# Kernel tuning notes

Measured on AMD Instinct MI355X. Metric: run time of the kernel, lower is better.

Reference implementation:

```python
import jax, jax.numpy as jnp
import numpy as np

N = 50000
IN_CHNL = 128
OUT_CHNL = 64
HEADS = 2
NEG_SLOPE = 0.2  # PyG GATConv default leaky_relu slope


def gat_conv(x, W, a_src, a_dst, bias, edge_index):
    """PyG-style GATConv (concat=True, add_self_loops=True, eval mode).
    x: [N, F_in], W: [F_in, H*C], a_src/a_dst: [H, C], bias: [H*C],
    edge_index: [2, E] (row 0 = src, row 1 = dst)."""
    n = x.shape[0]
    loops = jnp.arange(n, dtype=edge_index.dtype)
    src = jnp.concatenate([edge_index[0], loops])
    dst = jnp.concatenate([edge_index[1], loops])

    h = (x @ W).reshape(n, HEADS, OUT_CHNL)          # [N, H, C]
    s_src = jnp.einsum('nhc,hc->nh', h, a_src)       # [N, H]
    s_dst = jnp.einsum('nhc,hc->nh', h, a_dst)       # [N, H]

    e = s_src[src] + s_dst[dst]                      # [E', H]
    e = jax.nn.leaky_relu(e, NEG_SLOPE)
    # segment softmax over destination neighborhoods
    e_max = jax.ops.segment_max(e, dst, num_segments=n)
    e_max = jnp.where(jnp.isfinite(e_max), e_max, 0.0)
    e_exp = jnp.exp(e - e_max[dst])
    denom = jax.ops.segment_sum(e_exp, dst, num_segments=n)
    alpha = e_exp / denom[dst]                       # [E', H]

    msg = h[src] * alpha[:, :, None]                 # [E', H, C]
    out = jax.ops.segment_sum(msg, dst, num_segments=n)  # [N, H, C]
    return out.reshape(n, HEADS * OUT_CHNL) + bias


def setup_inputs() -> dict:
    key = jax.random.key(0)
    ks = jax.random.split(key, 12)
    node_h = jax.random.normal(ks[0], (N, IN_CHNL), dtype=jnp.float32)
    edge_index_pc = jax.random.randint(ks[1], (2, 600000), 0, N, dtype=jnp.int64 if jax.config.jax_enable_x64 else jnp.int32)
    edge_index_mc = jax.random.randint(ks[2], (2, 600000), 0, N, dtype=jnp.int64 if jax.config.jax_enable_x64 else jnp.int32)
    sc = 1.0 / np.sqrt(IN_CHNL)
    W_pc = jax.random.normal(ks[3], (IN_CHNL, HEADS * OUT_CHNL), dtype=jnp.float32) * sc
    a_src_pc = jax.random.normal(ks[4], (HEADS, OUT_CHNL), dtype=jnp.float32) * sc
    a_dst_pc = jax.random.normal(ks[5], (HEADS, OUT_CHNL), dtype=jnp.float32) * sc
    b_pc = jnp.zeros((HEADS * OUT_CHNL,), dtype=jnp.float32)
    W_mc = jax.random.normal(ks[6], (IN_CHNL, HEADS * OUT_CHNL), dtype=jnp.float32) * sc
    a_src_mc = jax.random.normal(ks[7], (HEADS, OUT_CHNL), dtype=jnp.float32) * sc
    a_dst_mc = jax.random.normal(ks[8], (HEADS, OUT_CHNL), dtype=jnp.float32) * sc
    b_mc = jnp.zeros((HEADS * OUT_CHNL,), dtype=jnp.float32)
    return {
        'node_h': node_h,
        'W_pc': W_pc, 'a_src_pc': a_src_pc, 'a_dst_pc': a_dst_pc, 'b_pc': b_pc,
        'W_mc': W_mc, 'a_src_mc': a_src_mc, 'a_dst_mc': a_dst_mc, 'b_mc': b_mc,
        'edge_index_pc': edge_index_pc, 'edge_index_mc': edge_index_mc,
    }


def reference(node_h, W_pc, a_src_pc, a_dst_pc, b_pc,
              W_mc, a_src_mc, a_dst_mc, b_mc,
              edge_index_pc, edge_index_mc):
    # eval mode: F.dropout is identity
    h_pc = jax.nn.elu(gat_conv(node_h, W_pc, a_src_pc, a_dst_pc, b_pc, edge_index_pc))
    h_mc = jax.nn.elu(gat_conv(node_h, W_mc, a_src_mc, a_dst_mc, b_mc, edge_index_mc))
    return 0.5 * (h_pc + h_mc)
```

## Files before the change

### kernel.cpp

```cpp
#include <hip/hip_runtime.h>
#include <hip/hip_bf16.h>

typedef unsigned int u32;
typedef unsigned short u16;
typedef long long i64;
typedef __bf16 bf16x8 __attribute__((ext_vector_type(8)));
typedef float f32x4 __attribute__((ext_vector_type(4)));

static constexpr int NN = 50000;
static constexpr int FI = 128;
static constexpr int FO = 128;
static constexpr int ER = 600000;
static constexpr int GLAB = 6272;
static constexpr int PROWS = 12544;
static constexpr int DSTRIDE = 38;
static constexpr int NQA = 1280;
static constexpr int ACS = (2 * ER + NQA - 1) / NQA;
static constexpr int NBIN = 128;
static constexpr int RBLK = 784;
static constexpr int LCAP = 24;
static constexpr int QCAPB = 10240;
static constexpr int GEMM_BLK = (NN + 63) / 64;
static constexpr int NGEMM = 2 * GEMM_BLK;
static constexpr float SLOPE = 0.2f;

__device__ __forceinline__ float bf2f(u16 u) {
  u32 x = ((u32)u) << 16;
  return __builtin_bit_cast(float, x);
}
__device__ __forceinline__ u16 f2bf(float f) {
  u32 u = __builtin_bit_cast(u32, f);
  u32 r = (u + 0x7fffu + ((u >> 16) & 1u)) >> 16;
  return (u16)r;
}
__device__ __forceinline__ float ldf(const void* p, size_t i, int isf32) {
  return isf32 ? ((const float*)p)[i] : bf2f(((const u16*)p)[i]);
}
__device__ __forceinline__ int lde(const void* p, size_t i, int is64) {
  return is64 ? (int)((const i64*)p)[i] : ((const int*)p)[i];
}

__global__ void wfrag_prep(const void* __restrict__ W0,
                           const void* __restrict__ W1,
                           const u32* __restrict__ x,
                           const u32* __restrict__ ei, u16* __restrict__ wf,
                           int* __restrict__ flags, int* __restrict__ qcurp) {
  int lane = threadIdx.x;
  u32 e = (x[lane] >> 23) & 0xffu;
  unsigned long long b1 = __ballot(e >= 118u && e <= 137u);
  int f32i = (__popcll(b1) >= 48) ? 1 : 0;
  int bid = blockIdx.x;
  if (bid == 64) {
    u32 hi = (lane < 32) ? ei[2 * lane + 1] : 1u;
    unsigned long long b2 = __ballot(hi == 0u);
    if (lane == 0) {
      flags[0] = f32i;
      flags[1] = (__popcll(b2) >= 30) ? 1 : 0;
    }
    for (int i = lane; i < NBIN * 16; i += 64) qcurp[i] = 0;
    return;
  }
  int g = bid >> 5, idx = bid & 31;
  const void* W = g ? W1 : W0;
  int ks = idx >> 3, cg = idx & 7;
  int k0 = ks * 32 + (lane >> 4) * 8;
  int col = cg * 16 + (lane & 15);
  u16 v[8];
#pragma unroll
  for (int j = 0; j < 8; j++) v[j] = f2bf(ldf(W, (size_t)(k0 + j) * FO + col, f32i));
  u32 p0 = (u32)v[0] | ((u32)v[1] << 16);
  u32 p1 = (u32)v[2] | ((u32)v[3] << 16);
  u32 p2 = (u32)v[4] | ((u32)v[5] << 16);
  u32 p3 = (u32)v[6] | ((u32)v[7] << 16);
  *reinterpret_cast<uint4*>(wf + (size_t)(bid * 64 + lane) * 8) =
      make_uint4(p0, p1, p2, p3);
}

__device__ __forceinline__ void passA_body(const void* __restrict__ ei0,
                                           const void* __restrict__ ei1,
                                           int* __restrict__ qcurp,
                                           u32* __restrict__ qbuf, int bid) {
  __shared__ u32 lq[NBIN][LCAP];
  __shared__ int lcnt[NBIN];
  __shared__ int gbase[NBIN];
  __shared__ int s_i64;
  int tid = threadIdx.x;
  if (tid < NBIN) lcnt[tid] = 0;
  if (tid < 64) {
    u32 hi = (tid < 32) ? ((const u32*)ei0)[2 * tid + 1] : 1u;
    unsigned long long b2 = __ballot(hi == 0u);
    if (tid == 0) s_i64 = (__popcll(b2) >= 30) ? 1 : 0;
  }
  __syncthreads();
  int i64f = s_i64;
  int beg = bid * ACS;
  int end = min(beg + ACS, 2 * ER);
  for (int e = beg + tid; e < end; e += 256) {
    int g = e >= ER;
    int ee = e - g * ER;
    const void* ei = g ? ei1 : ei0;
    int d = lde(ei, (size_t)ER + ee, i64f);
    int s = lde(ei, (size_t)ee, i64f);
    s = min(max(s, 0), NN - 1);
    d = min(max(d, 0), NN - 1);
    int p = d & 7;
    int label = (d >> 3) + g * GLAB;
    int r = label / RBLK;
    int bin = p * 16 + r;
    int ll = label - r * RBLK;
    u32 entry = ((u32)s << 16) | (u32)ll;
    int pos = atomicAdd(&lcnt[bin], 1);
    if (pos < LCAP) {
      lq[bin][pos] = entry;
    } else {
      int idx = atomicAdd(&qcurp[bin * 16], 1);
      if (idx < QCAPB) qbuf[(size_t)bin * QCAPB + idx] = entry;
    }
  }
  __syncthreads();
  if (tid < NBIN) {
    int n = min(lcnt[tid], LCAP);
    lcnt[tid] = n;
    gbase[tid] = atomicAdd(&qcurp[tid * 16], n);
  }
  __syncthreads();
  int wv = tid >> 6, lane = tid & 63;
  for (int b = wv; b < NBIN; b += 4) {
    int n = lcnt[b];
    int gb = gbase[b];
    for (int i = lane; i < n; i += 64) {
      int idx = gb + i;
      if (idx < QCAPB) qbuf[(size_t)b * QCAPB + idx] = lq[b][i];
    }
  }
}

__device__ __forceinline__ void gemm_body(
    const void* __restrict__ x, const u16* __restrict__ wf,
    u16* __restrict__ h0, u16* __restrict__ h1, const void* __restrict__ as0,
    const void* __restrict__ ad0, const void* __restrict__ as1,
    const void* __restrict__ ad1, float* __restrict__ ss,
    float* __restrict__ sd, int f32i, int gb) {
  int g = gb >= GEMM_BLK;
  int bid = gb - g * GEMM_BLK;
  u16* h = g ? h1 : h0;
  const void* as = g ? as1 : as0;
  const void* ad = g ? ad1 : ad0;
  int tid = threadIdx.x;
  int lane = tid & 63, wv = tid >> 6;
  int rowbase = bid * 64 + wv * 16;
  int arow = rowbase + (lane & 15);
  if (arow >= NN) arow = NN - 1;
  int kg = lane >> 4;

  f32x4 acc[8];
#pragma unroll
  for (int i = 0; i < 8; i++) acc[i] = (f32x4){0.f, 0.f, 0.f, 0.f};

#pragma unroll
  for (int ks = 0; ks < 4; ks++) {
    uint4 q;
    if (f32i) {
      const float* xp = (const float*)x + (size_t)arow * FI + ks * 32 + kg * 8;
      float4 v0 = *reinterpret_cast<const float4*>(xp);
      float4 v1 = *reinterpret_cast<const float4*>(xp + 4);
      q.x = (u32)f2bf(v0.x) | ((u32)f2bf(v0.y) << 16);
      q.y = (u32)f2bf(v0.z) | ((u32)f2bf(v0.w) << 16);
      q.z = (u32)f2bf(v1.x) | ((u32)f2bf(v1.y) << 16);
      q.w = (u32)f2bf(v1.z) | ((u32)f2bf(v1.w) << 16);
    } else {
      q = *reinterpret_cast<const uint4*>((const u16*)x + (size_t)arow * FI +
                                          ks * 32 + kg * 8);
    }
    bf16x8 a = __builtin_bit_cast(bf16x8, q);
#pragma unroll
    for (int cg = 0; cg < 8; cg++) {
      bf16x8 b = __builtin_bit_cast(
          bf16x8, *reinterpret_cast<const uint4*>(
                      wf + (size_t)((g * 32 + ks * 8 + cg) * 64 + lane) * 8));
      acc[cg] = __builtin_amdgcn_mfma_f32_16x16x32_bf16(a, b, acc[cg], 0, 0, 0);
    }
  }
#pragma unroll
  for (int cg = 0; cg < 8; cg++) {
#pragma unroll
    for (int r = 0; r < 4; r++) {
      int orow = rowbase + kg * 4 + r;
      if (orow < NN)
        h[(size_t)orow * FO + cg * 16 + (lane & 15)] = f2bf(acc[cg][r]);
    }
  }
  float sa[2][4], sb[2][4];
#pragma unroll
  for (int i = 0; i < 2; i++)
#pragma unroll
    for (int r = 0; r < 4; r++) {
      sa[i][r] = 0.f;
      sb[i][r] = 0.f;
    }
#pragma unroll
  for (int cg = 0; cg < 8; cg++) {
    int c = cg * 16 + (lane & 15);
    float av = ldf(as, c, f32i);
    float dv = ldf(ad, c, f32i);
    int ih = cg >> 2;
#pragma unroll
    for (int r = 0; r < 4; r++) {
      sa[ih][r] += acc[cg][r] * av;
      sb[ih][r] += acc[cg][r] * dv;
    }
  }
#pragma unroll
  for (int i = 0; i < 2; i++)
#pragma unroll
    for (int r = 0; r < 4; r++)
#pragma unroll
      for (int off = 1; off <= 8; off <<= 1) {
        sa[i][r] += __shfl_xor(sa[i][r], off, 64);
        sb[i][r] += __shfl_xor(sb[i][r], off, 64);
      }
  if ((lane & 15) < 4) {
    int r = lane & 3;
    int row = rowbase + kg * 4 + r;
    if (row < NN) {
      reinterpret_cast<float2*>(ss)[(size_t)g * NN + row] =
          make_float2(sa[0][r], sa[1][r]);
      reinterpret_cast<float2*>(sd)[(size_t)g * NN + row] =
          make_float2(sb[0][r], sb[1][r]);
    }
  }
}

__global__ __launch_bounds__(256) void fat1(
    const void* __restrict__ x, const u16* __restrict__ wf,
    u16* __restrict__ h0, u16* __restrict__ h1, const void* __restrict__ as0,
    const void* __restrict__ ad0, const void* __restrict__ as1,
    const void* __restrict__ ad1, float* __restrict__ ss,
    float* __restrict__ sd, const void* __restrict__ ei0,
    const void* __restrict__ ei1, int* __restrict__ qcurp,
    u32* __restrict__ qbuf, const int* __restrict__ flags) {
  if (blockIdx.x < NGEMM) {
    gemm_body(x, wf, h0, h1, as0, ad0, as1, ad1, ss, sd, flags[0],
              blockIdx.x);
  } else {
    passA_body(ei0, ei1, qcurp, qbuf, blockIdx.x - NGEMM);
  }
}

__global__ __launch_bounds__(256) void passB(const int* __restrict__ qcurp,
                                             const u32* __restrict__ qbuf,
                                             int* __restrict__ deg,
                                             u16* __restrict__ slots) {
  __shared__ int ldeg[RBLK];
  __shared__ u16 lslots[RBLK * DSTRIDE];
  int tid = threadIdx.x;
  int bin = blockIdx.x;
  int p = bin >> 4, r = bin & 15;
  for (int i = tid; i < RBLK; i += 256) {
    int lgl = r * RBLK + i;
    int g = lgl >= GLAB;
    int lg = lgl - g * GLAB;
    int dst = (lg << 3) | p;
    if (dst < NN) {
      ldeg[i] = 1;
      lslots[i * DSTRIDE] = (u16)dst;
    } else {
      ldeg[i] = 0;
    }
  }
  __syncthreads();
  int qn = min(qcurp[bin * 16], QCAPB);
  const u32* q = qbuf + (size_t)bin * QCAPB;
  for (int i = tid; i < qn; i += 256) {
    u32 pr = q[i];
    int ll = (int)(pr & 0xffffu);
    int old = atomicAdd(&ldeg[ll], 1);
    if (old < DSTRIDE) lslots[ll * DSTRIDE + old] = (u16)(pr >> 16);
  }
  __syncthreads();
  int rowbase = p * PROWS + r * RBLK;
  for (int i = tid; i < RBLK; i += 256) deg[rowbase + i] = min(ldeg[i], DSTRIDE);
  const u32* ls32 = reinterpret_cast<const u32*>(lslots);
  u32* gs32 = reinterpret_cast<u32*>(slots + (size_t)rowbase * DSTRIDE);
  for (int i = tid; i < RBLK * DSTRIDE / 2; i += 256) gs32[i] = ls32[i];
}

__global__ __launch_bounds__(256) void agg2(
    const u16* __restrict__ h0, const u16* __restrict__ h1,
    const float* __restrict__ ss, const float* __restrict__ sd,
    const int* __restrict__ deg, const u16* __restrict__ slots,
    const void* __restrict__ b0p, const void* __restrict__ b1p,
    void* __restrict__ outp, const int* __restrict__ flags) {
  int f32i = flags[0];
  int tid = threadIdx.x;
  int lane = tid & 63, wv = tid >> 6;
  int half = lane >> 5;
  int c = lane & 31;
  int dst = blockIdx.x * 8 + wv * 2 + half;
  int head = c >> 4;
  int hsh = head << 4;
  int hbase = half << 5;
  float res[2][4];
#pragma unroll
  for (int g = 0; g < 2; g++) {
    const uint2* hw = reinterpret_cast<const uint2*>(g ? h1 : h0);
    const float2* ss2 = reinterpret_cast<const float2*>(ss) + (size_t)g * NN;
    float2 sdv = reinterpret_cast<const float2*>(sd)[(size_t)g * NN + dst];
    int row = (dst & 7) * PROWS + g * GLAB + (dst >> 3);
    int n = min(deg[row], DSTRIDE);
    const u16* srow = slots + (size_t)row * DSTRIDE;
    int n1 = min(n, 32);
    int s1 = 0, s2 = 0;
    u32 pp1 = 0, pp2 = 0;
    float dp0 = 0.f, dp1 = 0.f;
    if (c < n1) {
      s1 = srow[c];
      float2 sv = ss2[s1];
      float e0 = sv.x + sdv.x, e1 = sv.y + sdv.y;
      e0 = (e0 > 0.f) ? e0 : SLOPE * e0;
      e1 = (e1 > 0.f) ? e1 : SLOPE * e1;
      float q0 = __expf(e0), q1 = __expf(e1);
      pp1 = (u32)f2bf(q0) | ((u32)f2bf(q1) << 16);
      dp0 += q0;
      dp1 += q1;
    }
    if (c + 32 < n) {
      s2 = srow[c + 32];
      float2 sv = ss2[s2];
      float e0 = sv.x + sdv.x, e1 = sv.y + sdv.y;
      e0 = (e0 > 0.f) ? e0 : SLOPE * e0;
      e1 = (e1 > 0.f) ? e1 : SLOPE * e1;
      float q0 = __expf(e0), q1 = __expf(e1);
      pp2 = (u32)f2bf(q0) | ((u32)f2bf(q1) << 16);
      dp0 += q0;
      dp1 += q1;
    }
#pragma unroll
    for (int off = 16; off >= 1; off >>= 1) {
      dp0 += __shfl_xor(dp0, off, 32);
      dp1 += __shfl_xor(dp1, off, 32);
    }
    float den = head ? dp1 : dp0;
    float a0 = 0.f, a1 = 0.f, a2 = 0.f, a3 = 0.f;
    int n1full = n1 & ~7;
    for (int b = 0; b < n1full; b += 8) {
      uint2 hv[8];
      float pv[8];
#pragma unroll
      for (int t = 0; t < 8; t++) {
        int sj = __shfl(s1, hbase + b + t, 64);
        u32 pp = __shfl(pp1, hbase + b + t, 64);
        pv[t] = bf2f((u16)(pp >> hsh));
        hv[t] = hw[(size_t)sj * 32 + c];
      }
#pragma unroll
      for (int t = 0; t < 8; t++) {
        a0 += pv[t] * bf2f((u16)hv[t].x);
        a1 += pv[t] * bf2f((u16)(hv[t].x >> 16));
        a2 += pv[t] * bf2f((u16)hv[t].y);
        a3 += pv[t] * bf2f((u16)(hv[t].y >> 16));
      }
    }
    if (n1full < n1) {
      uint2 hv[8];
      float pv[8];
#pragma unroll
      for (int t = 0; t < 8; t++) {
        int jj = (n1full + t < n1) ? (n1full + t) : n1full;
        int sj = __shfl(s1, hbase + jj, 64);
        u32 pp = __shfl(pp1, hbase + jj, 64);
        pv[t] = (n1full + t < n1) ? bf2f((u16)(pp >> hsh)) : 0.f;
        hv[t] = hw[(size_t)sj * 32 + c];
      }
#pragma unroll
      for (int t = 0; t < 8; t++) {
        a0 += pv[t] * bf2f((u16)hv[t].x);
        a1 += pv[t] * bf2f((u16)(hv[t].x >> 16));
        a2 += pv[t] * bf2f((u16)hv[t].y);
        a3 += pv[t] * bf2f((u16)(hv[t].y >> 16));
      }
    }
    if (n > 32) {
      int n2 = n - 32;
      for (int b = 0; b < n2; b += 8) {
        uint2 hv[8];
        float pv[8];
#pragma unroll
        for (int t = 0; t < 8; t++) {
          int jj = (b + t < n2) ? (b + t) : b;
          int sj = __shfl(s2, hbase + jj, 64);
          u32 pp = __shfl(pp2, hbase + jj, 64);
          pv[t] = (b + t < n2) ? bf2f((u16)(pp >> hsh)) : 0.f;
          hv[t] = hw[(size_t)sj * 32 + c];
        }
#pragma unroll
        for (int t = 0; t < 8; t++) {
          a0 += pv[t] * bf2f((u16)hv[t].x);
          a1 += pv[t] * bf2f((u16)(hv[t].x >> 16));
          a2 += pv[t] * bf2f((u16)hv[t].y);
          a3 += pv[t] * bf2f((u16)(hv[t].y >> 16));
        }
      }
    }
    float inv = (den > 0.f) ? 1.0f / den : 0.f;
    const void* bias = g ? b1p : b0p;
    float r0 = a0 * inv + ldf(bias, 4 * c + 0, f32i);
    float r1 = a1 * inv + ldf(bias, 4 * c + 1, f32i);
    float r2 = a2 * inv + ldf(bias, 4 * c + 2, f32i);
    float r3 = a3 * inv + ldf(bias, 4 * c + 3, f32i);
    res[g][0] = (r0 > 0.f) ? r0 : (__expf(r0) - 1.0f);
    res[g][1] = (r1 > 0.f) ? r1 : (__expf(r1) - 1.0f);
    res[g][2] = (r2 > 0.f) ? r2 : (__expf(r2) - 1.0f);
    res[g][3] = (r3 > 0.f) ? r3 : (__expf(r3) - 1.0f);
  }
  float r0 = 0.5f * (res[0][0] + res[1][0]);
  float r1 = 0.5f * (res[0][1] + res[1][1]);
  float r2 = 0.5f * (res[0][2] + res[1][2]);
  float r3 = 0.5f * (res[0][3] + res[1][3]);
  if (f32i) {
    reinterpret_cast<float4*>(outp)[(size_t)dst * 32 + c] =
        make_float4(r0, r1, r2, r3);
  } else {
    uint2 o;
    o.x = (u32)f2bf(r0) | ((u32)f2bf(r1) << 16);
    o.y = (u32)f2bf(r2) | ((u32)f2bf(r3) << 16);
    reinterpret_cast<uint2*>(outp)[(size_t)dst * 32 + c] = o;
  }
}

extern "C" void kernel_launch(void* const* d_in, const int* in_sizes, int n_in,
                              void* d_out, int out_size, void* d_ws, size_t ws_size,
                              hipStream_t stream) {
  (void)in_sizes; (void)n_in; (void)out_size; (void)ws_size;
  const void* x = d_in[0];

  char* base = (char*)d_ws;
  size_t off = 0;
  auto alloc = [&](size_t bytes) -> void* {
    void* p = base + off;
    off = (off + bytes + 255) & ~(size_t)255;
    return p;
  };
  int* flags = (int*)alloc(16);
  int* qcurp = (int*)alloc((size_t)NBIN * 16 * 4);
  u16* h0    = (u16*)alloc((size_t)NN * FO * 2);
  u16* h1    = (u16*)alloc((size_t)NN * FO * 2);
  float* ss  = (float*)alloc((size_t)2 * NN * 2 * 4);
  float* sd  = (float*)alloc((size_t)2 * NN * 2 * 4);
  u16* wf    = (u16*)alloc((size_t)2 * 32 * 64 * 8 * 2);
  int* deg   = (int*)alloc((size_t)8 * PROWS * 4);
  u16* slots = (u16*)alloc((size_t)8 * PROWS * DSTRIDE * 2);
  u32* qbuf  = (u32*)alloc((size_t)NBIN * QCAPB * 4);

  const int AGG_BLK = NN / 8;

  wfrag_prep<<<65, 64, 0, stream>>>(d_in[1], d_in[5], (const u32*)x,
                                    (const u32*)d_in[9], wf, flags, qcurp);
  fat1<<<NGEMM + NQA, 256, 0, stream>>>(x, wf, h0, h1, d_in[2], d_in[3],
                                        d_in[6], d_in[7], ss, sd, d_in[9],
                                        d_in[10], qcurp, qbuf, flags);
  passB<<<NBIN, 256, 0, stream>>>(qcurp, qbuf, deg, slots);
  agg2<<<AGG_BLK, 256, 0, stream>>>(h0, h1, ss, sd, deg, slots, d_in[4],
                                    d_in[8], d_out, flags);
}
```

Before: 130.5 us.

## Store h in column-permuted layout with vectorized 16-byte writes, unpermute in aggregation

The GEMM epilogue now writes each output row of h as one packed 16-byte store per lane, which permutes the column order of h, instead of scattering eight separate 2-byte stores. The aggregation kernel adapts to that layout: head selection becomes c&1, bias columns are remapped, and the final results go through shared memory to restore the original column order before the coalesced output store. This is meant to cut scattered write traffic in the GEMM, at the cost of an LDS round-trip per output row in the aggregation kernel.

```diff
diff --git a/kernel.cpp b/kernel.cpp
--- a/kernel.cpp
+++ b/kernel.cpp
@@ -23,6 +23,7 @@
 static constexpr int GEMM_BLK = (NN + 63) / 64;
 static constexpr int NGEMM = 2 * GEMM_BLK;
 static constexpr float SLOPE = 0.2f;
+
 
 __device__ __forceinline__ float bf2f(u16 u) {
   u32 x = ((u32)u) << 16;
@@ -181,13 +182,20 @@
       acc[cg] = __builtin_amdgcn_mfma_f32_16x16x32_bf16(a, b, acc[cg], 0, 0, 0);
     }
   }
-#pragma unroll
-  for (int cg = 0; cg < 8; cg++) {
-#pragma unroll
-    for (int r = 0; r < 4; r++) {
-      int orow = rowbase + kg * 4 + r;
-      if (orow < NN)
-        h[(size_t)orow * FO + cg * 16 + (lane & 15)] = f2bf(acc[cg][r]);
+  int c15 = lane & 15;
+#pragma unroll
+  for (int r = 0; r < 4; r++) {
+    int orow = rowbase + kg * 4 + r;
+    if (orow < NN) {
+      u16 v[8];
+#pragma unroll
+      for (int cg = 0; cg < 8; cg++) v[cg] = f2bf(acc[cg][r]);
+      uint4 q4;
+      q4.x = (u32)v[0] | ((u32)v[1] << 16);
+      q4.y = (u32)v[2] | ((u32)v[3] << 16);
+      q4.z = (u32)v[4] | ((u32)v[5] << 16);
+      q4.w = (u32)v[6] | ((u32)v[7] << 16);
+      *reinterpret_cast<uint4*>(h + (size_t)orow * FO + c15 * 8) = q4;
     }
   }
   float sa[2][4], sb[2][4];
@@ -200,7 +208,7 @@
     }
 #pragma unroll
   for (int cg = 0; cg < 8; cg++) {
-    int c = cg * 16 + (lane & 15);
+    int c = cg * 16 + c15;
     float av = ldf(as, c, f32i);
     float dv = ldf(ad, c, f32i);
     int ih = cg >> 2;
@@ -219,7 +227,7 @@
         sa[i][r] += __shfl_xor(sa[i][r], off, 64);
         sb[i][r] += __shfl_xor(sb[i][r], off, 64);
       }
-  if ((lane & 15) < 4) {
+  if (c15 < 4) {
     int r = lane & 3;
     int row = rowbase + kg * 4 + r;
     if (row < NN) {
@@ -291,13 +299,14 @@
     const int* __restrict__ deg, const u16* __restrict__ slots,
     const void* __restrict__ b0p, const void* __restrict__ b1p,
     void* __restrict__ outp, const int* __restrict__ flags) {
+  __shared__ float xbuf[4][2][128];
   int f32i = flags[0];
   int tid = threadIdx.x;
   int lane = tid & 63, wv = tid >> 6;
   int half = lane >> 5;
   int c = lane & 31;
   int dst = blockIdx.x * 8 + wv * 2 + half;
-  int head = c >> 4;
+  int head = c & 1;
   int hsh = head << 4;
   int hbase = half << 5;
   float res[2][4];
@@ -404,26 +413,34 @@
     }
     float inv = (den > 0.f) ? 1.0f / den : 0.f;
     const void* bias = g ? b1p : b0p;
-    float r0 = a0 * inv + ldf(bias, 4 * c + 0, f32i);
-    float r1 = a1 * inv + ldf(bias, 4 * c + 1, f32i);
-    float r2 = a2 * inv + ldf(bias, 4 * c + 2, f32i);
-    float r3 = a3 * inv + ldf(bias, 4 * c + 3, f32i);
-    res[g][0] = (r0 > 0.f) ? r0 : (__expf(r0) - 1.0f);
-    res[g][1] = (r1 > 0.f) ? r1 : (__expf(r1) - 1.0f);
-    res[g][2] = (r2 > 0.f) ? r2 : (__expf(r2) - 1.0f);
-    res[g][3] = (r3 > 0.f) ? r3 : (__expf(r3) - 1.0f);
-  }
-  float r0 = 0.5f * (res[0][0] + res[1][0]);
-  float r1 = 0.5f * (res[0][1] + res[1][1]);
-  float r2 = 0.5f * (res[0][2] + res[1][2]);
-  float r3 = 0.5f * (res[0][3] + res[1][3]);
+    float aa[4] = {a0, a1, a2, a3};
+#pragma unroll
+    for (int j = 0; j < 4; j++) {
+      int col = (4 * (c & 1) + j) * 16 + (c >> 1);
+      float rr = aa[j] * inv + ldf(bias, col, f32i);
+      res[g][j] = (rr > 0.f) ? rr : (__expf(rr) - 1.0f);
+    }
+  }
+  float* xb = &xbuf[wv][half][0];
+  float4 fq;
+  fq.x = 0.5f * (res[0][0] + res[1][0]);
+  fq.y = 0.5f * (res[0][1] + res[1][1]);
+  fq.z = 0.5f * (res[0][2] + res[1][2]);
+  fq.w = 0.5f * (res[0][3] + res[1][3]);
+  reinterpret_cast<float4*>(xb)[c] = fq;
+  float cf[4];
+#pragma unroll
+  for (int j = 0; j < 4; j++) {
+    int q = 4 * c + j;
+    cf[j] = xb[((q & 15) << 3) | (q >> 4)];
+  }
   if (f32i) {
     reinterpret_cast<float4*>(outp)[(size_t)dst * 32 + c] =
-        make_float4(r0, r1, r2, r3);
+        make_float4(cf[0], cf[1], cf[2], cf[3]);
   } else {
     uint2 o;
-    o.x = (u32)f2bf(r0) | ((u32)f2bf(r1) << 16);
-    o.y = (u32)f2bf(r2) | ((u32)f2bf(r3) << 16);
+    o.x = (u32)f2bf(cf[0]) | ((u32)f2bf(cf[1]) << 16);
+    o.y = (u32)f2bf(cf[2]) | ((u32)f2bf(cf[3]) << 16);
     reinterpret_cast<uint2*>(outp)[(size_t)dst * 32 + c] = o;
   }
 }
```

After: 131.7 us. Within noise of the previous version (+0.9%).
